# Performance work log

Hardware: AMD Instinct MI355X
Metric: run time of the kernel (lower is better)

Reference implementation:

```python
import jax, jax.numpy as jnp
import numpy as np

N = 100000      # num nodes
E = 800000      # num edges
IN = 256        # in_features
D = 64          # out_features per head
H = 4           # num_heads
EF = 64         # edge_feats
NET = 8         # num_etype
SLOPE = 0.2     # leaky relu negative slope


def setup_inputs() -> dict:
    key = jax.random.key(0)
    ks = jax.random.split(key, 12)
    s = 0.05
    h = jax.random.normal(ks[0], (N, IN), jnp.float32)
    row = jax.random.randint(ks[1], (E,), 0, N, dtype=jnp.int32)   # src
    col = jax.random.randint(ks[2], (E,), 0, N, dtype=jnp.int32)   # dst
    tp = jax.random.randint(ks[3], (E,), 0, NET, dtype=jnp.int32)  # edge type
    W = jax.random.normal(ks[4], (IN, D * H), jnp.float32) * s
    W_e = jax.random.normal(ks[5], (EF, EF * H), jnp.float32) * s
    edge_emb = jax.random.normal(ks[6], (NET, EF), jnp.float32) * s
    a_l = jax.random.normal(ks[7], (1, H, D), jnp.float32) * s
    a_r = jax.random.normal(ks[8], (1, H, D), jnp.float32) * s
    a_e = jax.random.normal(ks[9], (1, H, EF), jnp.float32) * s
    res_W = jax.random.normal(ks[10], (IN, D * H), jnp.float32) * s
    res_b = jnp.zeros((D * H,), jnp.float32)
    return {"h": h, "W": W, "W_e": W_e, "edge_emb": edge_emb,
            "a_l": a_l, "a_r": a_r, "a_e": a_e,
            "res_W": res_W, "res_b": res_b,
            "row": row, "col": col, "tp": tp}


def reference(h, W, W_e, edge_emb, a_l, a_r, a_e, res_W, res_b, row, col, tp):
    # node projection -> [N, H, D]; nan-guard as in the original
    emb = jnp.nan_to_num((h @ W).reshape(-1, H, D), nan=0.0)
    # edge-type embedding projection -> [NET, H, EF]
    e = (edge_emb @ W_e).reshape(-1, H, EF)
    # per-edge attention logits [E, H]
    h_l = (a_l * emb).sum(-1)[row]
    h_r = (a_r * emb).sum(-1)[col]
    h_e = (a_e * e).sum(-1)[tp]
    att = jax.nn.leaky_relu(h_l + h_r + h_e, SLOPE)
    # segment softmax over edges grouped by destination node
    m = jax.ops.segment_max(att, col, num_segments=N)          # [N, H]
    ex = jnp.exp(att - m[col])                                 # [E, H]
    denom = jax.ops.segment_sum(ex, col, num_segments=N)      # [N, H]
    alpha = ex / denom[col]                                    # [E, H]
    # gather-multiply-scatter message passing: [E, H, D] -> [N, H, D]
    msg = emb[row] * alpha[:, :, None]
    out = jax.ops.segment_sum(msg, col, num_segments=N).reshape(N, H * D)
    # residual linear + elu activation
    out = out + h @ res_W + res_b
    return jax.nn.elu(out)
```

## Files before the change

### kernel.cpp

```cpp
#include <hip/hip_runtime.h>

#define N_NODES 100000
#define E_EDGES 800000
#define IN_F 256
#define D_HEAD 64
#define H_HEADS 4
#define EF_F 64
#define NET_T 8
#define HD 256
#define SLOPE 0.2f

typedef unsigned short u16;
typedef unsigned long long u64;
typedef __attribute__((ext_vector_type(8))) short bf16x8;
typedef __attribute__((ext_vector_type(4))) float f32x4;

static __device__ __forceinline__ u16 f2bf(float f) {
    unsigned int u = __float_as_uint(f);
    unsigned int r = u + 0x7FFFu + ((u >> 16) & 1u);
    return (u16)(r >> 16);
}
static __device__ __forceinline__ float bf2f(unsigned int u) {
    return __uint_as_float(u << 16);
}

__global__ void k_se(const float* __restrict__ edge_emb, const float* __restrict__ W_e,
                     const float* __restrict__ a_e, float* __restrict__ s_e) {
    int tid = threadIdx.x;
    int t  = tid >> 5;
    int h  = (tid >> 3) & 3;
    int fc = tid & 7;
    float part = 0.f;
    for (int j = 0; j < 8; ++j) {
        int f = fc * 8 + j;
        float acc = 0.f;
        for (int k = 0; k < EF_F; ++k)
            acc += edge_emb[t * EF_F + k] * W_e[k * (EF_F * H_HEADS) + h * EF_F + f];
        part += a_e[h * EF_F + f] * acc;
    }
    for (int off = 1; off < 8; off <<= 1)
        part += __shfl_xor(part, off, 64);
    if (fc == 0) s_e[t * H_HEADS + h] = part;
}

__global__ void k_prep_w(const float* __restrict__ W, const float* __restrict__ resW,
                         u16* __restrict__ Bt) {
    const int id = blockIdx.x * 256 + threadIdx.x;
    const int n = id >> 8;
    const int k = id & 255;
    const float v = (n < HD) ? W[k * HD + n] : resW[k * HD + (n - HD)];
    Bt[id] = f2bf(v);
}

__global__ __launch_bounds__(512, 2)
void k_mfma(const float* __restrict__ A, const u16* __restrict__ Bt,
            const float* __restrict__ a_l, const float* __restrict__ a_r,
            const float* __restrict__ resb,
            u16* __restrict__ emb_bf, float* __restrict__ s_l, float* __restrict__ s_r,
            float* __restrict__ outp) {
    __shared__ char At[32768];
    const int tid = threadIdx.x;
    const int lane = tid & 63;
    const int wid = tid >> 6;
    const int row0 = blockIdx.x * 64;

#pragma unroll
    for (int c = 0; c < 8; ++c) {
        const int lin8 = c * 4096 + tid * 8;
        const int r_lin = lin8 >> 9;
        int grow = row0 + r_lin;
        if (grow >= N_NODES) grow = N_NODES - 1;
        const int colb = lin8 & 511;
        const float4 v = *reinterpret_cast<const float4*>(&A[(size_t)grow * IN_F + (colb >> 1)]);
        uint2 o;
        o.x = (unsigned)f2bf(v.x) | ((unsigned)f2bf(v.y) << 16);
        o.y = (unsigned)f2bf(v.z) | ((unsigned)f2bf(v.w) << 16);
        *reinterpret_cast<uint2*>(&At[lin8 ^ ((r_lin & 7) << 4)]) = o;
    }
    __syncthreads();

    const int lr = lane & 15;
    const int lg = lane >> 4;
    const int xr = (lr & 7) << 4;
    const int klg = lg * 16;
    const int n0 = wid * 64;

    int rowbase[4];
#pragma unroll
    for (int m = 0; m < 4; ++m) rowbase[m] = (m * 16 + lr) * 512;

    f32x4 acc[4][4] = {};
#pragma unroll
    for (int ks = 0; ks < 8; ++ks) {
        const int koff = ks * 32 + klg / 2;
        bf16x8 af[4], bfr[4];
        const int kx = ((ks << 6) + klg) ^ xr;
#pragma unroll
        for (int m = 0; m < 4; ++m)
            af[m] = *reinterpret_cast<const bf16x8*>(&At[rowbase[m] + kx]);
#pragma unroll
        for (int n = 0; n < 4; ++n)
            bfr[n] = *reinterpret_cast<const bf16x8*>(&Bt[(size_t)(n0 + n * 16 + lr) * IN_F + koff]);
#pragma unroll
        for (int m = 0; m < 4; ++m)
#pragma unroll
            for (int n = 0; n < 4; ++n)
                acc[m][n] = __builtin_amdgcn_mfma_f32_16x16x32_bf16(af[m], bfr[n], acc[m][n], 0, 0, 0);
    }

    if (wid < 4) {
        const int h = wid;
        float alv[4], arv[4];
#pragma unroll
        for (int n = 0; n < 4; ++n) {
            alv[n] = a_l[h * D_HEAD + n * 16 + lr];
            arv[n] = a_r[h * D_HEAD + n * 16 + lr];
        }
#pragma unroll
        for (int m = 0; m < 4; ++m) {
#pragma unroll
            for (int r = 0; r < 4; ++r) {
                const int node = row0 + m * 16 + lg * 4 + r;
                float dl = 0.f, dr = 0.f;
                u16 pk[4];
#pragma unroll
                for (int n = 0; n < 4; ++n) {
                    float v = acc[m][n][r];
                    v = isnan(v) ? 0.f : v;
                    dl += v * alv[n];
                    dr += v * arv[n];
                    pk[n] = f2bf(v);
                }
                if (node < N_NODES) {
                    const size_t base = (size_t)node * HD + h * D_HEAD;
#pragma unroll
                    for (int n = 0; n < 4; ++n)
                        emb_bf[base + n * 16 + lr] = pk[n];
                }
                dl += __shfl_xor(dl, 1, 64); dr += __shfl_xor(dr, 1, 64);
                dl += __shfl_xor(dl, 2, 64); dr += __shfl_xor(dr, 2, 64);
                dl += __shfl_xor(dl, 4, 64); dr += __shfl_xor(dr, 4, 64);
                dl += __shfl_xor(dl, 8, 64); dr += __shfl_xor(dr, 8, 64);
                if (lr == 0 && node < N_NODES) {
                    s_l[node * H_HEADS + h] = dl;
                    s_r[node * H_HEADS + h] = dr;
                }
            }
        }
    } else {
        const int c0 = (wid - 4) * 64;
        float rb[4];
#pragma unroll
        for (int n = 0; n < 4; ++n) rb[n] = resb[c0 + n * 16 + lr];
#pragma unroll
        for (int m = 0; m < 4; ++m) {
#pragma unroll
            for (int r = 0; r < 4; ++r) {
                const int node = row0 + m * 16 + lg * 4 + r;
                if (node < N_NODES) {
                    const size_t base = (size_t)node * HD + c0;
#pragma unroll
                    for (int n = 0; n < 4; ++n)
                        outp[base + n * 16 + lr] = acc[m][n][r] + rb[n];
                }
            }
        }
    }
}

__global__ void k_hist(const int* __restrict__ col, int* __restrict__ counts) {
    int e = blockIdx.x * 256 + threadIdx.x;
    if (e < E_EDGES) atomicAdd(&counts[col[e]], 1);
}

__global__ void k_scan1(const int* __restrict__ counts, int* __restrict__ row_ptr,
                        int* __restrict__ partials) {
    __shared__ int sd[256];
    const int t = threadIdx.x, b = blockIdx.x;
    const int base = b * 1024 + t * 4;
    int v[4];
#pragma unroll
    for (int j = 0; j < 4; ++j) v[j] = (base + j < N_NODES) ? counts[base + j] : 0;
    const int s = v[0] + v[1] + v[2] + v[3];
    sd[t] = s;
    __syncthreads();
    for (int off = 1; off < 256; off <<= 1) {
        int y = (t >= off) ? sd[t - off] : 0;
        __syncthreads();
        sd[t] += y;
        __syncthreads();
    }
    int p = sd[t] - s;
#pragma unroll
    for (int j = 0; j < 4; ++j) {
        if (base + j < N_NODES) row_ptr[base + j] = p;
        p += v[j];
    }
    if (t == 255) partials[b] = sd[255];
}

__global__ void k_scan2(int* __restrict__ partials) {
    __shared__ int sd[128];
    const int t = threadIdx.x;
    const int v = (t < 98) ? partials[t] : 0;
    sd[t] = v;
    __syncthreads();
    for (int off = 1; off < 128; off <<= 1) {
        int y = (t >= off) ? sd[t - off] : 0;
        __syncthreads();
        sd[t] += y;
        __syncthreads();
    }
    if (t < 98) partials[t] = sd[t] - v;
}

__global__ void k_scan3(int* __restrict__ row_ptr, int* __restrict__ fill,
                        const int* __restrict__ partials) {
    const int i = blockIdx.x * 256 + threadIdx.x;
    if (i < N_NODES) {
        const int v = row_ptr[i] + partials[i >> 10];
        row_ptr[i] = v;
        fill[i] = v;
    }
    if (i == 0) row_ptr[N_NODES] = E_EDGES;
}

__global__ void k_scatter(const int* __restrict__ row, const int* __restrict__ col,
                          const int* __restrict__ tp, int* __restrict__ fill,
                          int* __restrict__ perm) {
    int e = blockIdx.x * 256 + threadIdx.x;
    if (e < E_EDGES) {
        int c = col[e];
        int p = atomicAdd(&fill[c], 1);
        perm[p] = row[e] | (tp[e] << 20);
    }
}

__global__ __launch_bounds__(256)
void k_aggregate(const int* __restrict__ row_ptr, const int* __restrict__ perm,
                 const u16* __restrict__ emb_bf, const float* __restrict__ s_l,
                 const float* __restrict__ s_r, const float* __restrict__ s_e,
                 float* __restrict__ outp) {
    const int wave = threadIdx.x >> 6;
    const int lane = threadIdx.x & 63;
    const int n = blockIdx.x * 4 + wave;
    const int h = lane >> 4;
    const int start = row_ptr[n], end = row_ptr[n + 1];
    const float srh = s_r[n * H_HEADS + h];

    float se_h[NET_T];
#pragma unroll
    for (int t = 0; t < NET_T; ++t) se_h[t] = s_e[t * H_HEADS + h];

    float a0 = 0.f, a1 = 0.f, a2 = 0.f, a3 = 0.f, den = 0.f;
    int i = start;
    for (; i + 2 <= end; i += 2) {
        const int p0 = perm[i], p1 = perm[i + 1];
        const int r0 = p0 & 0xFFFFF, r1 = p1 & 0xFFFFF;
        const u64 ev0 = *reinterpret_cast<const u64*>(&emb_bf[(size_t)r0 * HD + lane * 4]);
        const u64 ev1 = *reinterpret_cast<const u64*>(&emb_bf[(size_t)r1 * HD + lane * 4]);
        const float sl0 = s_l[r0 * H_HEADS + h];
        const float sl1 = s_l[r1 * H_HEADS + h];
        float lg0 = sl0 + srh + se_h[p0 >> 20];
        float lg1 = sl1 + srh + se_h[p1 >> 20];
        lg0 = (lg0 > 0.f) ? lg0 : SLOPE * lg0;
        lg1 = (lg1 > 0.f) ? lg1 : SLOPE * lg1;
        const float ex0 = __expf(lg0);
        const float ex1 = __expf(lg1);
        a0 += ex0 * bf2f((unsigned)(ev0) & 0xFFFFu)      + ex1 * bf2f((unsigned)(ev1) & 0xFFFFu);
        a1 += ex0 * bf2f((unsigned)(ev0 >> 16) & 0xFFFFu) + ex1 * bf2f((unsigned)(ev1 >> 16) & 0xFFFFu);
        a2 += ex0 * bf2f((unsigned)(ev0 >> 32) & 0xFFFFu) + ex1 * bf2f((unsigned)(ev1 >> 32) & 0xFFFFu);
        a3 += ex0 * bf2f((unsigned)(ev0 >> 48) & 0xFFFFu) + ex1 * bf2f((unsigned)(ev1 >> 48) & 0xFFFFu);
        den += ex0 + ex1;
    }
    if (i < end) {
        const int p0 = perm[i];
        const int r0 = p0 & 0xFFFFF;
        const u64 ev0 = *reinterpret_cast<const u64*>(&emb_bf[(size_t)r0 * HD + lane * 4]);
        float lg0 = s_l[r0 * H_HEADS + h] + srh + se_h[p0 >> 20];
        lg0 = (lg0 > 0.f) ? lg0 : SLOPE * lg0;
        const float ex0 = __expf(lg0);
        a0 += ex0 * bf2f((unsigned)(ev0) & 0xFFFFu);
        a1 += ex0 * bf2f((unsigned)(ev0 >> 16) & 0xFFFFu);
        a2 += ex0 * bf2f((unsigned)(ev0 >> 32) & 0xFFFFu);
        a3 += ex0 * bf2f((unsigned)(ev0 >> 48) & 0xFFFFu);
        den += ex0;
    }
    const float inv = (den > 0.f) ? 1.f / den : 0.f;
    const size_t o = (size_t)n * HD + lane * 4;
    float4 res = *reinterpret_cast<const float4*>(&outp[o]);
    float4 out;
    float x;
    x = a0 * inv + res.x; out.x = (x > 0.f) ? x : expm1f(x);
    x = a1 * inv + res.y; out.y = (x > 0.f) ? x : expm1f(x);
    x = a2 * inv + res.z; out.z = (x > 0.f) ? x : expm1f(x);
    x = a3 * inv + res.w; out.w = (x > 0.f) ? x : expm1f(x);
    *reinterpret_cast<float4*>(&outp[o]) = out;
}

extern "C" void kernel_launch(void* const* d_in, const int* in_sizes, int n_in,
                              void* d_out, int out_size, void* d_ws, size_t ws_size,
                              hipStream_t stream) {
    const float* h    = (const float*)d_in[0];
    const float* W    = (const float*)d_in[1];
    const float* W_e  = (const float*)d_in[2];
    const float* eemb = (const float*)d_in[3];
    const float* a_l  = (const float*)d_in[4];
    const float* a_r  = (const float*)d_in[5];
    const float* a_e  = (const float*)d_in[6];
    const float* resW = (const float*)d_in[7];
    const float* resb = (const float*)d_in[8];
    const int* row = (const int*)d_in[9];
    const int* col = (const int*)d_in[10];
    const int* tp  = (const int*)d_in[11];
    float* outp = (float*)d_out;

    char* ws = (char*)d_ws;
    size_t off = 0;
    auto alloc = [&](size_t b) { size_t o = off; off += (b + 255) & ~(size_t)255; return o; };
    u16*  Bt      = (u16*)(ws + alloc((size_t)512 * IN_F * 2));
    u16*  emb_bf  = (u16*)(ws + alloc((size_t)N_NODES * HD * 2));
    float* s_l    = (float*)(ws + alloc((size_t)N_NODES * H_HEADS * 4));
    float* s_r    = (float*)(ws + alloc((size_t)N_NODES * H_HEADS * 4));
    float* s_e    = (float*)(ws + alloc(NET_T * H_HEADS * 4));
    int*  counts  = (int*)(ws + alloc((size_t)N_NODES * 4));
    int*  row_ptr = (int*)(ws + alloc((size_t)(N_NODES + 1) * 4));
    int*  fill    = (int*)(ws + alloc((size_t)N_NODES * 4));
    int*  perm    = (int*)(ws + alloc((size_t)E_EDGES * 4));
    int*  partials= (int*)(ws + alloc(128 * 4));

    k_se<<<1, 256, 0, stream>>>(eemb, W_e, a_e, s_e);
    k_prep_w<<<512, 256, 0, stream>>>(W, resW, Bt);
    k_mfma<<<(N_NODES + 63) / 64, 512, 0, stream>>>(h, Bt, a_l, a_r, resb, emb_bf, s_l, s_r, outp);
    hipMemsetAsync(counts, 0, (size_t)N_NODES * 4, stream);
    k_hist<<<(E_EDGES + 255) / 256, 256, 0, stream>>>(col, counts);
    k_scan1<<<98, 256, 0, stream>>>(counts, row_ptr, partials);
    k_scan2<<<1, 128, 0, stream>>>(partials);
    k_scan3<<<(N_NODES + 255) / 256, 256, 0, stream>>>(row_ptr, fill, partials);
    k_scatter<<<(E_EDGES + 255) / 256, 256, 0, stream>>>(row, col, tp, fill, perm);
    k_aggregate<<<N_NODES / 4, 256, 0, stream>>>(row_ptr, perm, emb_bf, s_l, s_r, s_e, outp);
}
```

Baseline: 343.1 us.

## Pre-swizzle weights into MFMA fragment order, transpose output mapping, unroll aggregation by four

The weight prep kernel now writes the bf16 weights in per-lane MFMA fragment order, so each wave's B loads become fully contiguous 16-byte reads. The MFMA operands are swapped so each lane holds four consecutive output columns, which lets the epilogue store emb as 8-byte packed words and outp as float4. The logit reduction also needs fewer shuffles. Separately, the aggregation loop is unrolled to four edges with the residual load hoisted, to expose more independent gathers per wave, at the cost of more registers.

```diff
diff --git a/kernel.cpp b/kernel.cpp
--- a/kernel.cpp
+++ b/kernel.cpp
@@ -44,16 +44,26 @@
 }
 
 __global__ void k_prep_w(const float* __restrict__ W, const float* __restrict__ resW,
-                         u16* __restrict__ Bt) {
-    const int id = blockIdx.x * 256 + threadIdx.x;
-    const int n = id >> 8;
-    const int k = id & 255;
-    const float v = (n < HD) ? W[k * HD + n] : resW[k * HD + (n - HD)];
-    Bt[id] = f2bf(v);
+                         u16* __restrict__ Bfrag) {
+    const int gid = blockIdx.x * 256 + threadIdx.x;
+    const int lane = gid & 63;
+    const int fragid = gid >> 6;
+    const int n = fragid & 3;
+    const int ks = (fragid >> 2) & 7;
+    const int g = fragid >> 5;
+    const int c = g * 64 + n * 16 + (lane & 15);
+    const int k0 = ks * 32 + (lane >> 4) * 8;
+    const float* src = (c < HD) ? &W[c] : &resW[c - HD];
+    u16 tmp[8];
+#pragma unroll
+    for (int j = 0; j < 8; ++j)
+        tmp[j] = f2bf(src[(size_t)(k0 + j) * HD]);
+    *reinterpret_cast<uint4*>(&Bfrag[(size_t)fragid * 512 + lane * 8]) =
+        *reinterpret_cast<const uint4*>(tmp);
 }
 
 __global__ __launch_bounds__(512, 2)
-void k_mfma(const float* __restrict__ A, const u16* __restrict__ Bt,
+void k_mfma(const float* __restrict__ A, const u16* __restrict__ Bfrag,
             const float* __restrict__ a_l, const float* __restrict__ a_r,
             const float* __restrict__ resb,
             u16* __restrict__ emb_bf, float* __restrict__ s_l, float* __restrict__ s_r,
@@ -83,85 +93,88 @@
     const int lg = lane >> 4;
     const int xr = (lr & 7) << 4;
     const int klg = lg * 16;
-    const int n0 = wid * 64;
 
     int rowbase[4];
 #pragma unroll
     for (int m = 0; m < 4; ++m) rowbase[m] = (m * 16 + lr) * 512;
 
+    const u16* bp = Bfrag + (size_t)wid * 16384 + lane * 8;
+
     f32x4 acc[4][4] = {};
 #pragma unroll
     for (int ks = 0; ks < 8; ++ks) {
-        const int koff = ks * 32 + klg / 2;
         bf16x8 af[4], bfr[4];
         const int kx = ((ks << 6) + klg) ^ xr;
 #pragma unroll
+        for (int n = 0; n < 4; ++n)
+            bfr[n] = *reinterpret_cast<const bf16x8*>(&bp[ks * 2048 + n * 512]);
+#pragma unroll
         for (int m = 0; m < 4; ++m)
             af[m] = *reinterpret_cast<const bf16x8*>(&At[rowbase[m] + kx]);
 #pragma unroll
-        for (int n = 0; n < 4; ++n)
-            bfr[n] = *reinterpret_cast<const bf16x8*>(&Bt[(size_t)(n0 + n * 16 + lr) * IN_F + koff]);
-#pragma unroll
         for (int m = 0; m < 4; ++m)
 #pragma unroll
             for (int n = 0; n < 4; ++n)
-                acc[m][n] = __builtin_amdgcn_mfma_f32_16x16x32_bf16(af[m], bfr[n], acc[m][n], 0, 0, 0);
+                acc[m][n] = __builtin_amdgcn_mfma_f32_16x16x32_bf16(bfr[n], af[m], acc[m][n], 0, 0, 0);
     }
 
     if (wid < 4) {
         const int h = wid;
-        float alv[4], arv[4];
+        float4 alv[4], arv[4];
 #pragma unroll
         for (int n = 0; n < 4; ++n) {
-            alv[n] = a_l[h * D_HEAD + n * 16 + lr];
-            arv[n] = a_r[h * D_HEAD + n * 16 + lr];
+            alv[n] = *reinterpret_cast<const float4*>(&a_l[h * D_HEAD + n * 16 + lg * 4]);
+            arv[n] = *reinterpret_cast<const float4*>(&a_r[h * D_HEAD + n * 16 + lg * 4]);
         }
 #pragma unroll
         for (int m = 0; m < 4; ++m) {
-#pragma unroll
-            for (int r = 0; r < 4; ++r) {
-                const int node = row0 + m * 16 + lg * 4 + r;
-                float dl = 0.f, dr = 0.f;
-                u16 pk[4];
-#pragma unroll
-                for (int n = 0; n < 4; ++n) {
-                    float v = acc[m][n][r];
-                    v = isnan(v) ? 0.f : v;
-                    dl += v * alv[n];
-                    dr += v * arv[n];
-                    pk[n] = f2bf(v);
-                }
-                if (node < N_NODES) {
-                    const size_t base = (size_t)node * HD + h * D_HEAD;
-#pragma unroll
-                    for (int n = 0; n < 4; ++n)
-                        emb_bf[base + n * 16 + lr] = pk[n];
-                }
-                dl += __shfl_xor(dl, 1, 64); dr += __shfl_xor(dr, 1, 64);
-                dl += __shfl_xor(dl, 2, 64); dr += __shfl_xor(dr, 2, 64);
-                dl += __shfl_xor(dl, 4, 64); dr += __shfl_xor(dr, 4, 64);
-                dl += __shfl_xor(dl, 8, 64); dr += __shfl_xor(dr, 8, 64);
-                if (lr == 0 && node < N_NODES) {
-                    s_l[node * H_HEADS + h] = dl;
-                    s_r[node * H_HEADS + h] = dr;
-                }
+            const int node = row0 + m * 16 + lr;
+            float dl = 0.f, dr = 0.f;
+            u64 pk[4];
+#pragma unroll
+            for (int n = 0; n < 4; ++n) {
+                float v0 = acc[m][n][0], v1 = acc[m][n][1], v2 = acc[m][n][2], v3 = acc[m][n][3];
+                v0 = isnan(v0) ? 0.f : v0;
+                v1 = isnan(v1) ? 0.f : v1;
+                v2 = isnan(v2) ? 0.f : v2;
+                v3 = isnan(v3) ? 0.f : v3;
+                dl += v0 * alv[n].x + v1 * alv[n].y + v2 * alv[n].z + v3 * alv[n].w;
+                dr += v0 * arv[n].x + v1 * arv[n].y + v2 * arv[n].z + v3 * arv[n].w;
+                pk[n] = (u64)f2bf(v0) | ((u64)f2bf(v1) << 16) |
+                        ((u64)f2bf(v2) << 32) | ((u64)f2bf(v3) << 48);
+            }
+            if (node < N_NODES) {
+                const size_t base = (size_t)node * HD + h * D_HEAD + lg * 4;
+#pragma unroll
+                for (int n = 0; n < 4; ++n)
+                    *reinterpret_cast<u64*>(&emb_bf[base + n * 16]) = pk[n];
+            }
+            dl += __shfl_xor(dl, 16, 64); dr += __shfl_xor(dr, 16, 64);
+            dl += __shfl_xor(dl, 32, 64); dr += __shfl_xor(dr, 32, 64);
+            if (lg == 0 && node < N_NODES) {
+                s_l[node * H_HEADS + h] = dl;
+                s_r[node * H_HEADS + h] = dr;
             }
         }
     } else {
-        const int c0 = (wid - 4) * 64;
-        float rb[4];
-#pragma unroll
-        for (int n = 0; n < 4; ++n) rb[n] = resb[c0 + n * 16 + lr];
+        const int c0 = (wid - 4) * 64 + lg * 4;
+        float4 rb[4];
+#pragma unroll
+        for (int n = 0; n < 4; ++n)
+            rb[n] = *reinterpret_cast<const float4*>(&resb[c0 + n * 16]);
 #pragma unroll
         for (int m = 0; m < 4; ++m) {
-#pragma unroll
-            for (int r = 0; r < 4; ++r) {
-                const int node = row0 + m * 16 + lg * 4 + r;
-                if (node < N_NODES) {
-                    const size_t base = (size_t)node * HD + c0;
-#pragma unroll
-                    for (int n = 0; n < 4; ++n)
-                        outp[base + n * 16 + lr] = acc[m][n][r] + rb[n];
+            const int node = row0 + m * 16 + lr;
+            if (node < N_NODES) {
+                const size_t base = (size_t)node * HD + c0;
+#pragma unroll
+                for (int n = 0; n < 4; ++n) {
+                    float4 o;
+                    o.x = acc[m][n][0] + rb[n].x;
+                    o.y = acc[m][n][1] + rb[n].y;
+                    o.z = acc[m][n][2] + rb[n].z;
+                    o.w = acc[m][n][3] + rb[n].w;
+                    *reinterpret_cast<float4*>(&outp[base + n * 16]) = o;
                 }
             }
         }
@@ -247,6 +260,8 @@
     const int h = lane >> 4;
     const int start = row_ptr[n], end = row_ptr[n + 1];
     const float srh = s_r[n * H_HEADS + h];
+    const size_t o = (size_t)n * HD + lane * 4;
+    const float4 res = *reinterpret_cast<const float4*>(&outp[o]);
 
     float se_h[NET_T];
 #pragma unroll
@@ -254,26 +269,38 @@
 
     float a0 = 0.f, a1 = 0.f, a2 = 0.f, a3 = 0.f, den = 0.f;
     int i = start;
-    for (; i + 2 <= end; i += 2) {
-        const int p0 = perm[i], p1 = perm[i + 1];
-        const int r0 = p0 & 0xFFFFF, r1 = p1 & 0xFFFFF;
+    for (; i + 4 <= end; i += 4) {
+        const int p0 = perm[i], p1 = perm[i + 1], p2 = perm[i + 2], p3 = perm[i + 3];
+        const int r0 = p0 & 0xFFFFF, r1 = p1 & 0xFFFFF, r2 = p2 & 0xFFFFF, r3 = p3 & 0xFFFFF;
         const u64 ev0 = *reinterpret_cast<const u64*>(&emb_bf[(size_t)r0 * HD + lane * 4]);
         const u64 ev1 = *reinterpret_cast<const u64*>(&emb_bf[(size_t)r1 * HD + lane * 4]);
+        const u64 ev2 = *reinterpret_cast<const u64*>(&emb_bf[(size_t)r2 * HD + lane * 4]);
+        const u64 ev3 = *reinterpret_cast<const u64*>(&emb_bf[(size_t)r3 * HD + lane * 4]);
         const float sl0 = s_l[r0 * H_HEADS + h];
         const float sl1 = s_l[r1 * H_HEADS + h];
+        const float sl2 = s_l[r2 * H_HEADS + h];
+        const float sl3 = s_l[r3 * H_HEADS + h];
         float lg0 = sl0 + srh + se_h[p0 >> 20];
         float lg1 = sl1 + srh + se_h[p1 >> 20];
+        float lg2 = sl2 + srh + se_h[p2 >> 20];
+        float lg3 = sl3 + srh + se_h[p3 >> 20];
         lg0 = (lg0 > 0.f) ? lg0 : SLOPE * lg0;
         lg1 = (lg1 > 0.f) ? lg1 : SLOPE * lg1;
-        const float ex0 = __expf(lg0);
-        const float ex1 = __expf(lg1);
-        a0 += ex0 * bf2f((unsigned)(ev0) & 0xFFFFu)      + ex1 * bf2f((unsigned)(ev1) & 0xFFFFu);
-        a1 += ex0 * bf2f((unsigned)(ev0 >> 16) & 0xFFFFu) + ex1 * bf2f((unsigned)(ev1 >> 16) & 0xFFFFu);
-        a2 += ex0 * bf2f((unsigned)(ev0 >> 32) & 0xFFFFu) + ex1 * bf2f((unsigned)(ev1 >> 32) & 0xFFFFu);
-        a3 += ex0 * bf2f((unsigned)(ev0 >> 48) & 0xFFFFu) + ex1 * bf2f((unsigned)(ev1 >> 48) & 0xFFFFu);
-        den += ex0 + ex1;
-    }
-    if (i < end) {
+        lg2 = (lg2 > 0.f) ? lg2 : SLOPE * lg2;
+        lg3 = (lg3 > 0.f) ? lg3 : SLOPE * lg3;
+        const float ex0 = __expf(lg0), ex1 = __expf(lg1);
+        const float ex2 = __expf(lg2), ex3 = __expf(lg3);
+        a0 += ex0 * bf2f((unsigned)(ev0) & 0xFFFFu)       + ex1 * bf2f((unsigned)(ev1) & 0xFFFFu)
+            + ex2 * bf2f((unsigned)(ev2) & 0xFFFFu)       + ex3 * bf2f((unsigned)(ev3) & 0xFFFFu);
+        a1 += ex0 * bf2f((unsigned)(ev0 >> 16) & 0xFFFFu) + ex1 * bf2f((unsigned)(ev1 >> 16) & 0xFFFFu)
+            + ex2 * bf2f((unsigned)(ev2 >> 16) & 0xFFFFu) + ex3 * bf2f((unsigned)(ev3 >> 16) & 0xFFFFu);
+        a2 += ex0 * bf2f((unsigned)(ev0 >> 32) & 0xFFFFu) + ex1 * bf2f((unsigned)(ev1 >> 32) & 0xFFFFu)
+            + ex2 * bf2f((unsigned)(ev2 >> 32) & 0xFFFFu) + ex3 * bf2f((unsigned)(ev3 >> 32) & 0xFFFFu);
+        a3 += ex0 * bf2f((unsigned)(ev0 >> 48) & 0xFFFFu) + ex1 * bf2f((unsigned)(ev1 >> 48) & 0xFFFFu)
+            + ex2 * bf2f((unsigned)(ev2 >> 48) & 0xFFFFu) + ex3 * bf2f((unsigned)(ev3 >> 48) & 0xFFFFu);
+        den += ex0 + ex1 + ex2 + ex3;
+    }
+    for (; i < end; ++i) {
         const int p0 = perm[i];
         const int r0 = p0 & 0xFFFFF;
         const u64 ev0 = *reinterpret_cast<const u64*>(&emb_bf[(size_t)r0 * HD + lane * 4]);
@@ -287,8 +314,6 @@
         den += ex0;
     }
     const float inv = (den > 0.f) ? 1.f / den : 0.f;
-    const size_t o = (size_t)n * HD + lane * 4;
-    float4 res = *reinterpret_cast<const float4*>(&outp[o]);
     float4 out;
     float x;
     x = a0 * inv + res.x; out.x = (x > 0.f) ? x : expm1f(x);
@@ -318,7 +343,7 @@
     char* ws = (char*)d_ws;
     size_t off = 0;
     auto alloc = [&](size_t b) { size_t o = off; off += (b + 255) & ~(size_t)255; return o; };
-    u16*  Bt      = (u16*)(ws + alloc((size_t)512 * IN_F * 2));
+    u16*  Bfrag   = (u16*)(ws + alloc((size_t)512 * IN_F * 2));
     u16*  emb_bf  = (u16*)(ws + alloc((size_t)N_NODES * HD * 2));
     float* s_l    = (float*)(ws + alloc((size_t)N_NODES * H_HEADS * 4));
     float* s_r    = (float*)(ws + alloc((size_t)N_NODES * H_HEADS * 4));
@@ -330,8 +355,8 @@
     int*  partials= (int*)(ws + alloc(128 * 4));
 
     k_se<<<1, 256, 0, stream>>>(eemb, W_e, a_e, s_e);
-    k_prep_w<<<512, 256, 0, stream>>>(W, resW, Bt);
-    k_mfma<<<(N_NODES + 63) / 64, 512, 0, stream>>>(h, Bt, a_l, a_r, resb, emb_bf, s_l, s_r, outp);
+    k_prep_w<<<64, 256, 0, stream>>>(W, resW, Bfrag);
+    k_mfma<<<(N_NODES + 63) / 64, 512, 0, stream>>>(h, Bfrag, a_l, a_r, resb, emb_bf, s_l, s_r, outp);
     hipMemsetAsync(counts, 0, (size_t)N_NODES * 4, stream);
     k_hist<<<(E_EDGES + 255) / 256, 256, 0, stream>>>(col, counts);
     k_scan1<<<98, 256, 0, stream>>>(counts, row_ptr, partials);
```

Result: faster. 322.6 us (-6.0%).
